# Kernel optimization log

Measured on AMD Instinct MI355X. Metric: run time of the kernel, lower is better.

## Reference

```python
import jax, jax.numpy as jnp
import numpy as np

B, T, SD, AD, H, K, HID = 256, 128, 8, 2, 3, 4, 256


def setup_inputs() -> dict:
    key = jax.random.key(0)
    ks = jax.random.split(key, 12)
    inp = {
        "state": jax.random.normal(ks[0], (B, T, SD), dtype=jnp.float32),
        "action": jax.random.normal(ks[1], (B, T, AD), dtype=jnp.float32),
        # Linear(4, 4*H, bias=False): weight (4*H, 4)
        "Wk": jax.random.normal(ks[2], (4 * H, K), dtype=jnp.float32) * 0.1,
        "Wq": jax.random.normal(ks[3], (4 * H, SD + AD), dtype=jnp.float32) * 0.1,
        "Wv": jax.random.normal(ks[4], (4 * H, K), dtype=jnp.float32) * 0.1,
        # MLP: in_dim = 4*H + SD + AD -> HID -> HID -> 1
        "W1": jax.random.normal(ks[5], (HID, 4 * H + SD + AD), dtype=jnp.float32) * 0.05,
        "b1": jnp.zeros((HID,), dtype=jnp.float32),
        "W2": jax.random.normal(ks[6], (HID, HID), dtype=jnp.float32) * 0.05,
        "b2": jnp.zeros((HID,), dtype=jnp.float32),
        "Wout": jax.random.uniform(ks[7], (1, HID), minval=-0.003, maxval=0.003, dtype=jnp.float32),
        "bout": jax.random.uniform(ks[8], (1,), minval=-0.003, maxval=0.003, dtype=jnp.float32),
    }
    return inp


def reference(state, action, Wk, Wq, Wv, W1, b1, W2, b2, Wout, bout):
    q_state = jnp.concatenate([state, action], axis=-1)  # (b, t, sd+ad)
    s = state[:, :, :4]                                   # (b, t, 4)
    b, t, k = s.shape
    h = Wk.shape[0] // k
    # rel_full[b, i, j] = s[b, j] - s[b, i]  (matches torch view/transpose)
    rel_full = s[:, None, :, :] - s[:, :, None, :]        # (b, t, t, 4)
    # drop diagonal (self-pairs): idx[i] = all j != i, in order
    j = jnp.arange(t - 1)
    idx = j[None, :] + (j[None, :] >= jnp.arange(t)[:, None])  # (t, t-1)
    rel = jnp.take_along_axis(rel_full, idx[None, :, :, None], axis=2)  # (b, t, t-1, 4)
    # QKV projections (tiny head dim k=4)
    q = (q_state @ Wq.T).reshape(b, t, h, k)              # (b, t, h, 4)
    keys = (rel @ Wk.T).reshape(b, t, t - 1, h, k)        # (b, t, t-1, h, 4)
    vals = (rel @ Wv.T).reshape(b, t, t - 1, h, k)
    scores = jnp.einsum('bthk,btjhk->bthj', q, keys) / jnp.sqrt(jnp.float32(k))
    w = jax.nn.softmax(scores, axis=-1)                   # over the t-1 neighbors
    x = jnp.einsum('bthj,btjhk->bthk', w, vals).reshape(b, t, h * k)
    x = jnp.concatenate([x, q_state], axis=-1)            # (b, t, h*4 + sd+ad)
    x = jax.nn.relu(x @ W1.T + b1)
    x = jax.nn.relu(x @ W2.T + b2)
    return x @ Wout.T + bout                              # (b, t, 1)
```

## Files before the change

### kernel.cpp

```cpp
#include <hip/hip_runtime.h>
#include <math.h>

#define Bp 256
#define Tp 128
#define SDp 8
#define ADp 2
#define Hp 3
#define Kp 4
#define HIDp 256
#define QDp (SDp + ADp)
#define X1Dp (Hp * Kp + QDp)
#define QKLD 20
#define LOG2E 1.4426950408889634f

typedef short bf16x8 __attribute__((ext_vector_type(8)));
typedef float f32x4  __attribute__((ext_vector_type(4)));

__device__ __forceinline__ unsigned short f2bf(float f) {
    unsigned u = __float_as_uint(f);
    unsigned r = (u + 0x7FFFu + ((u >> 16) & 1u)) >> 16;
    return (unsigned short)r;
}

__device__ __forceinline__ unsigned h1_byte(int row, int colbytes) {
    return (((unsigned)row << 9) + (unsigned)colbytes) ^ ((unsigned)(row & 7) << 4);
}

__global__ __launch_bounds__(256, 4) void attn_prep_kernel(
    const float* __restrict__ state, const float* __restrict__ action,
    const float* __restrict__ Wk, const float* __restrict__ Wq,
    const float* __restrict__ Wv, const float* __restrict__ W1,
    const float* __restrict__ W2, unsigned short* __restrict__ W1b,
    unsigned short* __restrict__ W2b, unsigned short* __restrict__ X1b)
{
    const int tid = threadIdx.x;
    if (blockIdx.x >= 1024) {
        const int pb = blockIdx.x - 1024;
        if (pb < 64) {
            const int i = pb * 1024 + tid * 4;
            const float4 v = *(const float4*)(W2 + i);
            ushort4 o;
            o.x = f2bf(v.x); o.y = f2bf(v.y); o.z = f2bf(v.z); o.w = f2bf(v.w);
            *(ushort4*)(W2b + i) = o;
        } else {
            const int i = (pb - 64) * 256 + tid;
            const int r = i >> 5, c = i & 31;
            W1b[i] = (c < X1Dp) ? f2bf(W1[r * X1Dp + c]) : (unsigned short)0;
        }
        return;
    }

    const int bid   = blockIdx.x;
    const int batch = bid >> 2;
    const int t0    = (bid & 3) * 32;
    const int t_loc = tid >> 3;
    const int jo    = tid & 7;
    const int t     = t0 + t_loc;

    __shared__ float4 s4[Tp];
    __shared__ float  wq[Hp * Kp * QDp];
    __shared__ float  wk[Hp * Kp * Kp];
    __shared__ float  wv[Hp * Kp * Kp];
    __shared__ float  qk[32 * QKLD];

    if (tid < Tp)
        s4[tid] = ((const float4*)(state + (size_t)batch * Tp * SDp))[tid * 2];
    if (tid >= Tp && tid < Tp + Hp * Kp * QDp)
        wq[tid - Tp] = Wq[tid - Tp];
    if (tid < Hp * Kp * Kp) { wk[tid] = Wk[tid]; wv[tid] = Wv[tid]; }
    __syncthreads();

    if (tid < 32) {
        const int tt = t0 + tid;
        const float* srow = state + ((size_t)batch * Tp + tt) * SDp;
        float qs[QDp];
        {
            const float4 v0 = *(const float4*)srow;
            const float4 v1 = *(const float4*)(srow + 4);
            qs[0]=v0.x; qs[1]=v0.y; qs[2]=v0.z; qs[3]=v0.w;
            qs[4]=v1.x; qs[5]=v1.y; qs[6]=v1.z; qs[7]=v1.w;
            const float* arow = action + ((size_t)batch * Tp + tt) * ADp;
            qs[8] = arow[0]; qs[9] = arow[1];
        }
        float q[Hp * Kp];
        #pragma unroll
        for (int r = 0; r < Hp * Kp; ++r) {
            float a = 0.f;
            #pragma unroll
            for (int d = 0; d < QDp; ++d) a += qs[d] * wq[r * QDp + d];
            q[r] = a;
        }
        float* qrow = &qk[tid * QKLD];
        const float4 st = s4[tt];
        #pragma unroll
        for (int h = 0; h < Hp; ++h) {
            float p[4];
            #pragma unroll
            for (int c = 0; c < Kp; ++c) {
                float a = 0.f;
                #pragma unroll
                for (int k = 0; k < Kp; ++k) a += q[h * Kp + k] * wk[(h * Kp + k) * Kp + c];
                p[c] = 0.5f * LOG2E * a;
                qrow[h * 4 + c] = p[c];
            }
            qrow[12 + h] = st.x * p[0] + st.y * p[1] + st.z * p[2] + st.w * p[3];
        }
        #pragma unroll
        for (int i = 0; i < 5; ++i) {
            const unsigned u = (unsigned)f2bf(qs[2*i]) | ((unsigned)f2bf(qs[2*i+1]) << 16);
            qrow[15 + i] = __uint_as_float(u);
        }
    }
    __syncthreads();

    float rq[20];
    #pragma unroll
    for (int i = 0; i < 5; ++i)
        *(float4*)&rq[i * 4] = *(const float4*)&qk[t_loc * QKLD + i * 4];

    float l[Hp] = {0.f, 0.f, 0.f};
    float ac[Hp][4] = {};
    #pragma unroll
    for (int i = 0; i < 16; ++i) {
        const int j = (jo << 4) | ((i + jo) & 15);
        const float4 sj = s4[j];
        #pragma unroll
        for (int h = 0; h < Hp; ++h) {
            const float d = sj.x * rq[h*4] + sj.y * rq[h*4+1]
                          + sj.z * rq[h*4+2] + sj.w * rq[h*4+3] - rq[12 + h];
            const float e = (j == t) ? 0.f : __builtin_amdgcn_exp2f(d);
            l[h] += e;
            ac[h][0] += e * sj.x; ac[h][1] += e * sj.y;
            ac[h][2] += e * sj.z; ac[h][3] += e * sj.w;
        }
    }
    #pragma unroll
    for (int off = 1; off < 8; off <<= 1) {
        #pragma unroll
        for (int h = 0; h < Hp; ++h) {
            l[h] += __shfl_xor(l[h], off);
            #pragma unroll
            for (int c = 0; c < Kp; ++c) ac[h][c] += __shfl_xor(ac[h][c], off);
        }
    }

    if (jo == 0) {
        const float4 st = s4[t];
        unsigned short rowb[32] __attribute__((aligned(16)));
        #pragma unroll
        for (int h = 0; h < Hp; ++h) {
            const float inv = 1.f / l[h];
            const float rb0 = ac[h][0] * inv - st.x;
            const float rb1 = ac[h][1] * inv - st.y;
            const float rb2 = ac[h][2] * inv - st.z;
            const float rb3 = ac[h][3] * inv - st.w;
            #pragma unroll
            for (int k = 0; k < Kp; ++k) {
                const int r = h * Kp + k;
                rowb[r] = f2bf(rb0 * wv[r*4] + rb1 * wv[r*4+1] + rb2 * wv[r*4+2] + rb3 * wv[r*4+3]);
            }
        }
        #pragma unroll
        for (int i = 0; i < 5; ++i) {
            const unsigned u = __float_as_uint(rq[15 + i]);
            rowb[12 + 2*i] = (unsigned short)(u & 0xffffu);
            rowb[13 + 2*i] = (unsigned short)(u >> 16);
        }
        #pragma unroll
        for (int i = X1Dp; i < 32; ++i) rowb[i] = 0;

        uint4* dst = (uint4*)(X1b + ((size_t)batch * Tp + t) * 32);
        const uint4* srcv = (const uint4*)rowb;
        #pragma unroll
        for (int i = 0; i < 4; ++i) dst[i] = srcv[i];
    }
}

__global__ __launch_bounds__(256, 3) void mlp_kernel(
    const unsigned short* __restrict__ X1b, const unsigned short* __restrict__ W1b,
    const unsigned short* __restrict__ W2b,
    const float* __restrict__ b1, const float* __restrict__ b2,
    const float* __restrict__ Wout, const float* __restrict__ bout,
    float* __restrict__ out)
{
    const int tid  = threadIdx.x;
    const int lane = tid & 63;
    const int wave = tid >> 6;
    const int quad = lane >> 4;
    const int l16  = lane & 15;
    const int pos0 = blockIdx.x * 32;

    __shared__ __align__(16) unsigned short h1s[32 * 256];
    __shared__ float partial[4][32];

    {
        const int rt  = wave & 1;
        const int chh = wave >> 1;
        const bf16x8 afr = *(const bf16x8*)&X1b[((size_t)pos0 + rt * 16 + l16) * 32 + quad * 8];
        #pragma unroll
        for (int n8 = 0; n8 < 8; ++n8) {
            const int col = chh * 128 + n8 * 16 + l16;
            const bf16x8 bfr = *(const bf16x8*)&W1b[col * 32 + quad * 8];
            f32x4 acc = {0.f, 0.f, 0.f, 0.f};
            acc = __builtin_amdgcn_mfma_f32_16x16x32_bf16(afr, bfr, acc, 0, 0, 0);
            const float bb = b1[col];
            #pragma unroll
            for (int r = 0; r < 4; ++r) {
                const int row = rt * 16 + quad * 4 + r;
                *(unsigned short*)((char*)h1s + h1_byte(row, col * 2)) =
                    f2bf(fmaxf(acc[r] + bb, 0.f));
            }
        }
    }
    __syncthreads();

    bf16x8 A[2][8];
    #pragma unroll
    for (int rt2 = 0; rt2 < 2; ++rt2)
        #pragma unroll
        for (int ks = 0; ks < 8; ++ks)
            A[rt2][ks] = *(const bf16x8*)((const char*)h1s +
                           h1_byte(rt2 * 16 + l16, ks * 64 + quad * 16));

    float rsum[2][4] = {};
    #pragma unroll
    for (int i = 0; i < 4; ++i) {
        const int col = (wave * 4 + i) * 16 + l16;
        const unsigned short* wr = W2b + (size_t)col * HIDp + quad * 8;
        bf16x8 Bf[8];
        #pragma unroll
        for (int ks = 0; ks < 8; ++ks)
            Bf[ks] = *(const bf16x8*)(wr + ks * 32);
        const float bb = b2[col];
        const float wo = Wout[col];
        #pragma unroll
        for (int rt2 = 0; rt2 < 2; ++rt2) {
            f32x4 acc = {0.f, 0.f, 0.f, 0.f};
            #pragma unroll
            for (int ks = 0; ks < 8; ++ks)
                acc = __builtin_amdgcn_mfma_f32_16x16x32_bf16(A[rt2][ks], Bf[ks], acc, 0, 0, 0);
            #pragma unroll
            for (int r = 0; r < 4; ++r)
                rsum[rt2][r] += fmaxf(acc[r] + bb, 0.f) * wo;
        }
    }

    #pragma unroll
    for (int off = 1; off < 16; off <<= 1)
        #pragma unroll
        for (int rt2 = 0; rt2 < 2; ++rt2)
            #pragma unroll
            for (int r = 0; r < 4; ++r)
                rsum[rt2][r] += __shfl_xor(rsum[rt2][r], off);

    if (l16 == 0) {
        #pragma unroll
        for (int rt2 = 0; rt2 < 2; ++rt2)
            #pragma unroll
            for (int r = 0; r < 4; ++r)
                partial[wave][rt2 * 16 + quad * 4 + r] = rsum[rt2][r];
    }
    __syncthreads();

    if (tid < 32) {
        out[pos0 + tid] = partial[0][tid] + partial[1][tid]
                        + partial[2][tid] + partial[3][tid] + bout[0];
    }
}

extern "C" void kernel_launch(void* const* d_in, const int* in_sizes, int n_in,
                              void* d_out, int out_size, void* d_ws, size_t ws_size,
                              hipStream_t stream) {
    const float* state  = (const float*)d_in[0];
    const float* action = (const float*)d_in[1];
    const float* Wk     = (const float*)d_in[2];
    const float* Wq     = (const float*)d_in[3];
    const float* Wv     = (const float*)d_in[4];
    const float* W1     = (const float*)d_in[5];
    const float* b1     = (const float*)d_in[6];
    const float* W2     = (const float*)d_in[7];
    const float* b2     = (const float*)d_in[8];
    const float* Wout   = (const float*)d_in[9];
    const float* bout   = (const float*)d_in[10];
    float* out = (float*)d_out;

    char* ws = (char*)d_ws;
    unsigned short* W1b = (unsigned short*)(ws);
    unsigned short* W2b = (unsigned short*)(ws + 16384);
    unsigned short* X1b = (unsigned short*)(ws + 16384 + 131072);

    attn_prep_kernel<<<1024 + 96, 256, 0, stream>>>(state, action, Wk, Wq, Wv,
                                                    W1, W2, W1b, W2b, X1b);
    mlp_kernel<<<(Bp * Tp) / 32, 256, 0, stream>>>(X1b, W1b, W2b, b1, b2,
                                                   Wout, bout, out);
}
```

Before: 101.3 us.

## Fuse attention stage into MLP kernel via shared-memory X1 tile

Merges the attention/prep kernel and the MLP kernel into one kernel. Each block now computes its 32 attention rows and stores the bf16 X1 tile in swizzled shared memory rather than global workspace. The MLP then runs in the same block. The weight-conversion work moves to a small separate prep kernel launched first. This removes the global X1 round-trip and one dependent launch of the big work. In exchange, shared-memory use and register pressure per block rise, which may lower occupancy, and there is still a separate prep launch.

```diff
diff --git a/kernel.cpp b/kernel.cpp
--- a/kernel.cpp
+++ b/kernel.cpp
@@ -25,34 +25,46 @@
 __device__ __forceinline__ unsigned h1_byte(int row, int colbytes) {
     return (((unsigned)row << 9) + (unsigned)colbytes) ^ ((unsigned)(row & 7) << 4);
 }
-
-__global__ __launch_bounds__(256, 4) void attn_prep_kernel(
+__device__ __forceinline__ unsigned x1_byte(int row, int colbytes) {
+    return ((unsigned)row << 6) + ((unsigned)colbytes ^ (((unsigned)row & 6u) << 3));
+}
+
+__global__ __launch_bounds__(256) void prep_kernel(
+    const float* __restrict__ W1, const float* __restrict__ W2,
+    unsigned short* __restrict__ W1b, unsigned short* __restrict__ W2b)
+{
+    const int bid = blockIdx.x;
+    const int tid = threadIdx.x;
+    if (bid < 64) {
+        const int i = bid * 1024 + tid * 4;
+        const float4 v = *(const float4*)(W2 + i);
+        ushort4 o;
+        o.x = f2bf(v.x); o.y = f2bf(v.y); o.z = f2bf(v.z); o.w = f2bf(v.w);
+        *(ushort4*)(W2b + i) = o;
+    } else {
+        const int i = (bid - 64) * 256 + tid;
+        const int r = i >> 5, c = i & 31;
+        W1b[i] = (c < X1Dp) ? f2bf(W1[r * X1Dp + c]) : (unsigned short)0;
+    }
+}
+
+__global__ __launch_bounds__(256, 4) void main_kernel(
     const float* __restrict__ state, const float* __restrict__ action,
     const float* __restrict__ Wk, const float* __restrict__ Wq,
-    const float* __restrict__ Wv, const float* __restrict__ W1,
-    const float* __restrict__ W2, unsigned short* __restrict__ W1b,
-    unsigned short* __restrict__ W2b, unsigned short* __restrict__ X1b)
+    const float* __restrict__ Wv,
+    const unsigned short* __restrict__ W1b, const unsigned short* __restrict__ W2b,
+    const float* __restrict__ b1, const float* __restrict__ b2,
+    const float* __restrict__ Wout, const float* __restrict__ bout,
+    float* __restrict__ out)
 {
-    const int tid = threadIdx.x;
-    if (blockIdx.x >= 1024) {
-        const int pb = blockIdx.x - 1024;
-        if (pb < 64) {
-            const int i = pb * 1024 + tid * 4;
-            const float4 v = *(const float4*)(W2 + i);
-            ushort4 o;
-            o.x = f2bf(v.x); o.y = f2bf(v.y); o.z = f2bf(v.z); o.w = f2bf(v.w);
-            *(ushort4*)(W2b + i) = o;
-        } else {
-            const int i = (pb - 64) * 256 + tid;
-            const int r = i >> 5, c = i & 31;
-            W1b[i] = (c < X1Dp) ? f2bf(W1[r * X1Dp + c]) : (unsigned short)0;
-        }
-        return;
-    }
-
     const int bid   = blockIdx.x;
     const int batch = bid >> 2;
     const int t0    = (bid & 3) * 32;
+    const int tid   = threadIdx.x;
+    const int lane  = tid & 63;
+    const int wave  = tid >> 6;
+    const int quad  = lane >> 4;
+    const int l16   = lane & 15;
     const int t_loc = tid >> 3;
     const int jo    = tid & 7;
     const int t     = t0 + t_loc;
@@ -62,6 +74,9 @@
     __shared__ float  wk[Hp * Kp * Kp];
     __shared__ float  wv[Hp * Kp * Kp];
     __shared__ float  qk[32 * QKLD];
+    __shared__ __align__(16) unsigned short X1s[32 * 32];
+    __shared__ __align__(16) unsigned short h1s[32 * 256];
+    __shared__ float partial[4][32];
 
     if (tid < Tp)
         s4[tid] = ((const float4*)(state + (size_t)batch * Tp * SDp))[tid * 2];
@@ -169,34 +184,18 @@
         #pragma unroll
         for (int i = X1Dp; i < 32; ++i) rowb[i] = 0;
 
-        uint4* dst = (uint4*)(X1b + ((size_t)batch * Tp + t) * 32);
         const uint4* srcv = (const uint4*)rowb;
         #pragma unroll
-        for (int i = 0; i < 4; ++i) dst[i] = srcv[i];
-    }
-}
-
-__global__ __launch_bounds__(256, 3) void mlp_kernel(
-    const unsigned short* __restrict__ X1b, const unsigned short* __restrict__ W1b,
-    const unsigned short* __restrict__ W2b,
-    const float* __restrict__ b1, const float* __restrict__ b2,
-    const float* __restrict__ Wout, const float* __restrict__ bout,
-    float* __restrict__ out)
-{
-    const int tid  = threadIdx.x;
-    const int lane = tid & 63;
-    const int wave = tid >> 6;
-    const int quad = lane >> 4;
-    const int l16  = lane & 15;
-    const int pos0 = blockIdx.x * 32;
-
-    __shared__ __align__(16) unsigned short h1s[32 * 256];
-    __shared__ float partial[4][32];
+        for (int i = 0; i < 4; ++i)
+            *(uint4*)((char*)X1s + x1_byte(t_loc, i * 16)) = srcv[i];
+    }
+    __syncthreads();
 
     {
         const int rt  = wave & 1;
         const int chh = wave >> 1;
-        const bf16x8 afr = *(const bf16x8*)&X1b[((size_t)pos0 + rt * 16 + l16) * 32 + quad * 8];
+        const bf16x8 afr = *(const bf16x8*)((const char*)X1s +
+                             x1_byte(rt * 16 + l16, quad * 16));
         #pragma unroll
         for (int n8 = 0; n8 < 8; ++n8) {
             const int col = chh * 128 + n8 * 16 + l16;
@@ -263,8 +262,9 @@
     __syncthreads();
 
     if (tid < 32) {
-        out[pos0 + tid] = partial[0][tid] + partial[1][tid]
-                        + partial[2][tid] + partial[3][tid] + bout[0];
+        out[(size_t)batch * Tp + t0 + tid] =
+            partial[0][tid] + partial[1][tid] + partial[2][tid]
+          + partial[3][tid] + bout[0];
     }
 }
 
@@ -287,10 +287,8 @@
     char* ws = (char*)d_ws;
     unsigned short* W1b = (unsigned short*)(ws);
     unsigned short* W2b = (unsigned short*)(ws + 16384);
-    unsigned short* X1b = (unsigned short*)(ws + 16384 + 131072);
-
-    attn_prep_kernel<<<1024 + 96, 256, 0, stream>>>(state, action, Wk, Wq, Wv,
-                                                    W1, W2, W1b, W2b, X1b);
-    mlp_kernel<<<(Bp * Tp) / 32, 256, 0, stream>>>(X1b, W1b, W2b, b1, b2,
-                                                   Wout, bout, out);
-}
+
+    prep_kernel<<<96, 256, 0, stream>>>(W1, W2, W1b, W2b);
+    main_kernel<<<4 * Bp, 256, 0, stream>>>(state, action, Wk, Wq, Wv,
+                                            W1b, W2b, b1, b2, Wout, bout, out);
+}
```

After: 99.36 us. 1.02x faster.
